# Kernel tuning notes

Hardware: AMD Instinct MI355X
Metric: run time of the kernel (lower is better)

Reference implementation:

```python
import jax, jax.numpy as jnp
import numpy as np

IN_DIM = 128
OUT_DIM = 128
N_NODES = 10000
N_EDGES = 640000


def setup_inputs() -> dict:
    key = jax.random.key(0)
    ks = jax.random.split(key, 9)
    X = jax.random.normal(ks[0], (N_NODES, IN_DIM), dtype=jnp.float32)
    edge_index = jax.random.randint(ks[1], (2, N_EDGES), 0, N_NODES, dtype=jnp.int64)
    edge_types = jax.random.randint(ks[2], (N_EDGES,), 0, 2, dtype=jnp.int64)
    s = 1.0 / np.sqrt(IN_DIM)
    W_data = jax.random.uniform(ks[3], (OUT_DIM, IN_DIM), minval=-s, maxval=s, dtype=jnp.float32)
    b_data = jax.random.uniform(ks[4], (OUT_DIM,), minval=-s, maxval=s, dtype=jnp.float32)
    W_control = jax.random.uniform(ks[5], (OUT_DIM, IN_DIM), minval=-s, maxval=s, dtype=jnp.float32)
    b_control = jax.random.uniform(ks[6], (OUT_DIM,), minval=-s, maxval=s, dtype=jnp.float32)
    W_self = jax.random.uniform(ks[7], (OUT_DIM, IN_DIM), minval=-s, maxval=s, dtype=jnp.float32)
    b_self = jax.random.uniform(ks[8], (OUT_DIM,), minval=-s, maxval=s, dtype=jnp.float32)
    return {"X": X, "edge_index": edge_index, "edge_types": edge_types,
            "W_data": W_data, "b_data": b_data,
            "W_control": W_control, "b_control": b_control,
            "W_self": W_self, "b_self": b_self}


def reference(X, edge_index, edge_types, W_data, b_data, W_control, b_control, W_self, b_self):
    src, dst = edge_index[0], edge_index[1]
    Xs = X[src]                               # [E, in_dim] gather
    m_data = Xs @ W_data.T + b_data           # [E, out_dim]
    m_ctrl = Xs @ W_control.T + b_control     # [E, out_dim]
    msg = jnp.where((edge_types == 0)[:, None], m_data, m_ctrl)
    agg = jax.ops.segment_sum(msg, dst, num_segments=X.shape[0])  # scatter-add to dst
    out = agg + (X @ W_self.T + b_self)
    return jax.nn.relu(out)
```

## Files before the change

kernel.cpp:

```cpp
#include <hip/hip_runtime.h>


#define IN_DIM 128
#define K_CAT  384
#define CAP    256
#define CSTR   16
#define ROWP   392

typedef short short8  __attribute__((ext_vector_type(8)));
typedef float floatx4 __attribute__((ext_vector_type(4)));

#define NW_ITEMS (8 * 12 * 64)

__device__ inline unsigned short f2bf(float f) {
    unsigned u = __float_as_uint(f);
    u += 0x7FFF + ((u >> 16) & 1);
    return (unsigned short)(u >> 16);
}
__device__ inline float bu2f(unsigned short h) {
    return __uint_as_float(((unsigned)h) << 16);
}

__global__ __launch_bounds__(256) void prep_kernel(
    const float* __restrict__ X,
    const float* __restrict__ Wd, const float* __restrict__ Wc,
    const float* __restrict__ Ws,
    unsigned short* __restrict__ WB,
    unsigned short* __restrict__ Xb,
    int* __restrict__ cnt, int N)
{
    const int NX = N * 32;
    const int NC = N * CSTR / 4;
    int idx = blockIdx.x * 256 + threadIdx.x;

    if (idx < NW_ITEMS) {
        int lane = idx & 63;
        int kt   = (idx >> 6) % 12;
        int nt   = idx / (64 * 12);
        int col  = nt * 16 + (lane & 15);
        int kb   = kt * 32 + (lane >> 4) * 8;
        unsigned short v[8];
        #pragma unroll
        for (int j = 0; j < 8; j++) {
            int k = kb + j;
            float w = (k < 128) ? Wd[col * 128 + k]
                    : (k < 256) ? Wc[col * 128 + (k - 128)]
                                : Ws[col * 128 + (k - 256)];
            v[j] = f2bf(w);
        }
        *(short8*)(WB + (size_t)idx * 8) = *(short8*)v;
        return;
    }
    idx -= NW_ITEMS;
    if (idx < NX) {
        float4 v = ((const float4*)X)[idx];
        ushort4 o;
        o.x = f2bf(v.x); o.y = f2bf(v.y); o.z = f2bf(v.z); o.w = f2bf(v.w);
        ((ushort4*)Xb)[idx] = o;
        return;
    }
    idx -= NX;
    if (idx < NC) {
        ((int4*)cnt)[idx] = make_int4(0, 0, 0, 0);
    }
}

__global__ __launch_bounds__(256) void append_kernel(
    const int* __restrict__ src,
    const int* __restrict__ dst,
    const int* __restrict__ etype,
    int* __restrict__ cnt,
    unsigned short* __restrict__ bucket, int E)
{
    int e = blockIdx.x * 256 + threadIdx.x;
    if (e >= E) return;
    int d = dst[e];
    int pos = atomicAdd(&cnt[d * CSTR], 1);
    if (pos < CAP) {
        bucket[(size_t)d * CAP + pos] =
            (unsigned short)(src[e] | (etype[e] << 15));
    }
}

__global__ __launch_bounds__(512) void fused_kernel(
    const unsigned short* __restrict__ Xb,
    const int* __restrict__ cnt,
    const unsigned short* __restrict__ bucket,
    const unsigned short* __restrict__ WB,
    const float* __restrict__ bd, const float* __restrict__ bc,
    const float* __restrict__ bs,
    float* __restrict__ out, int N)
{
    __shared__ unsigned short Als[16][ROWP];
    __shared__ float lc0[16], lc1[16];

    const int tid = threadIdx.x;
    const int m0  = blockIdx.x * 16;

    {
        const int hw = tid >> 5;
        const int q  = tid & 31;
        const int d  = m0 + hw;
        if (d < N) {
            const ushort4* Xb4 = (const ushort4*)Xb;
            int len = cnt[d * CSTR];
            if (len > CAP) len = CAP;

            float4 a0 = make_float4(0.f, 0.f, 0.f, 0.f);
            float4 a1 = make_float4(0.f, 0.f, 0.f, 0.f);
            int n0 = 0;
            const unsigned short* bl = bucket + (size_t)d * CAP;

#define PROC(P) do {                                                     \
            int _p = (int)(P);                                           \
            int _s = _p & 0x7FFF;                                        \
            int _t = _p >> 15;                                           \
            ushort4 _u = Xb4[_s * 32 + q];                               \
            float _x = bu2f(_u.x), _y = bu2f(_u.y);                      \
            float _z = bu2f(_u.z), _w = bu2f(_u.w);                      \
            float _m0 = _t ? 0.f : 1.f;                                  \
            float _m1 = 1.f - _m0;                                       \
            a0.x = fmaf(_x, _m0, a0.x); a1.x = fmaf(_x, _m1, a1.x);      \
            a0.y = fmaf(_y, _m0, a0.y); a1.y = fmaf(_y, _m1, a1.y);      \
            a0.z = fmaf(_z, _m0, a0.z); a1.z = fmaf(_z, _m1, a1.z);      \
            a0.w = fmaf(_w, _m0, a0.w); a1.w = fmaf(_w, _m1, a1.w);      \
            n0 += 1 - _t;                                                \
        } while (0)
#define PROC8(PP) do {                                                   \
            PROC((PP).x & 0xFFFF); PROC((PP).x >> 16);                   \
            PROC((PP).y & 0xFFFF); PROC((PP).y >> 16);                   \
            PROC((PP).z & 0xFFFF); PROC((PP).z >> 16);                   \
            PROC((PP).w & 0xFFFF); PROC((PP).w >> 16);                   \
        } while (0)

            int i = 0;
            for (; i + 16 <= len; i += 16) {
                uint4 p0 = *(const uint4*)(bl + i);
                uint4 p1 = *(const uint4*)(bl + i + 8);
                PROC8(p0); PROC8(p1);
            }
            for (; i + 8 <= len; i += 8) {
                uint4 p0 = *(const uint4*)(bl + i);
                PROC8(p0);
            }
            for (; i < len; i++) PROC(bl[i]);
#undef PROC8
#undef PROC

            ushort4 ux = Xb4[d * 32 + q];
            unsigned short* row = &Als[hw][0];
            ushort4 o;
            o.x = f2bf(a0.x); o.y = f2bf(a0.y); o.z = f2bf(a0.z); o.w = f2bf(a0.w);
            *(ushort4*)(row + q * 4) = o;
            o.x = f2bf(a1.x); o.y = f2bf(a1.y); o.z = f2bf(a1.z); o.w = f2bf(a1.w);
            *(ushort4*)(row + 128 + q * 4) = o;
            *(ushort4*)(row + 256 + q * 4) = ux;
            if (q == 0) {
                lc0[hw] = (float)n0;
                lc1[hw] = (float)(len - n0);
            }
        }
    }
    __syncthreads();

    const int wave = tid >> 6;
    const int lane = tid & 63;
    const int rA   = lane & 15;
    const int quad = lane >> 4;

    floatx4 acc = (floatx4){0.f, 0.f, 0.f, 0.f};
    const short8* B8 = (const short8*)WB + (size_t)wave * 12 * 64 + lane;

    #pragma unroll
    for (int kt = 0; kt < 12; kt++) {
        short8 a = *(const short8*)&Als[rA][kt * 32 + quad * 8];
        short8 b = B8[kt * 64];
        acc = __builtin_amdgcn_mfma_f32_16x16x32_bf16(a, b, acc, 0, 0, 0);
    }

    const int col = wave * 16 + rA;
    const float bdv = bd[col], bcv = bc[col], bsv = bs[col];
    #pragma unroll
    for (int r = 0; r < 4; r++) {
        int lrow = quad * 4 + r;
        int grow = m0 + lrow;
        if (grow < N) {
            float v = acc[r] + lc0[lrow] * bdv + lc1[lrow] * bcv + bsv;
            out[(size_t)grow * 128 + col] = fmaxf(v, 0.f);
        }
    }
}

extern "C" void kernel_launch(void* const* d_in, const int* in_sizes, int n_in,
                              void* d_out, int out_size, void* d_ws, size_t ws_size,
                              hipStream_t stream) {
    const float* X  = (const float*)d_in[0];
    const int*   ei = (const int*)d_in[1];
    const int*   et = (const int*)d_in[2];
    const float* Wd = (const float*)d_in[3];
    const float* bd = (const float*)d_in[4];
    const float* Wc = (const float*)d_in[5];
    const float* bc = (const float*)d_in[6];
    const float* Ws = (const float*)d_in[7];
    const float* bs = (const float*)d_in[8];
    float* out = (float*)d_out;

    const int N = in_sizes[0] / IN_DIM;
    const int E = in_sizes[2];

    unsigned short* WB     = (unsigned short*)d_ws;
    unsigned short* Xb     = WB + (size_t)NW_ITEMS * 8;
    unsigned short* bucket = Xb + (size_t)N * IN_DIM;
    int*            cnt    = (int*)(bucket + (size_t)N * CAP);

    const int* src = ei;
    const int* dst = ei + E;

    int prep_items = NW_ITEMS + N * 32 + N * CSTR / 4;
    prep_kernel<<<(prep_items + 255) / 256, 256, 0, stream>>>(
        X, Wd, Wc, Ws, WB, Xb, cnt, N);

    int eb = (E + 255) / 256;
    append_kernel<<<eb, 256, 0, stream>>>(src, dst, et, cnt, bucket, E);

    int fb = (N + 15) / 16;
    fused_kernel<<<fb, 512, 0, stream>>>(Xb, cnt, bucket, WB, bd, bc, bs, out, N);
}
```

Before: 131.5 us.

## Split edge buckets by type and gather with per-type half-warps

Edges now go into two per-destination buckets, one per edge type, each with its own counter, so the gather no longer needs masked dual accumulation. Each destination row is handled by two 16-thread groups, one per type. Each thread loads 16 bytes (8 bf16 values) per neighbour and accumulates with plain adds. The append kernel handles four edges per thread using vectorized loads. The cost is twice the bucket memory and a separate counter per type. Bucket capacity now applies per type, so truncation behaviour differs from before.

```diff
diff --git a/kernel.cpp b/kernel.cpp
--- a/kernel.cpp
+++ b/kernel.cpp
@@ -8,6 +8,7 @@
 #define ROWP   392
 
 typedef short short8  __attribute__((ext_vector_type(8)));
+typedef unsigned short ushortx8 __attribute__((ext_vector_type(8)));
 typedef float floatx4 __attribute__((ext_vector_type(4)));
 
 #define NW_ITEMS (8 * 12 * 64)
@@ -16,9 +17,6 @@
     unsigned u = __float_as_uint(f);
     u += 0x7FFF + ((u >> 16) & 1);
     return (unsigned short)(u >> 16);
-}
-__device__ inline float bu2f(unsigned short h) {
-    return __uint_as_float(((unsigned)h) << 16);
 }
 
 __global__ __launch_bounds__(256) void prep_kernel(
@@ -70,22 +68,39 @@
     const int* __restrict__ dst,
     const int* __restrict__ etype,
     int* __restrict__ cnt,
-    unsigned short* __restrict__ bucket, int E)
+    unsigned short* __restrict__ b0,
+    unsigned short* __restrict__ b1, int E)
 {
-    int e = blockIdx.x * 256 + threadIdx.x;
-    if (e >= E) return;
-    int d = dst[e];
-    int pos = atomicAdd(&cnt[d * CSTR], 1);
-    if (pos < CAP) {
-        bucket[(size_t)d * CAP + pos] =
-            (unsigned short)(src[e] | (etype[e] << 15));
-    }
+    int e0 = (blockIdx.x * 256 + threadIdx.x) * 4;
+
+#define PUT(SS, DD, TT) do {                                             \
+        int _d = (DD); int _t = (TT);                                    \
+        unsigned short* _b = _t ? b1 : b0;                               \
+        int _pos = atomicAdd(&cnt[_d * CSTR + (_t << 3)], 1);            \
+        if (_pos < CAP)                                                  \
+            _b[(size_t)_d * CAP + _pos] = (unsigned short)(SS);          \
+    } while (0)
+
+    if (e0 + 4 <= E) {
+        int4 s = *(const int4*)(src + e0);
+        int4 d = *(const int4*)(dst + e0);
+        int4 t = *(const int4*)(etype + e0);
+        PUT(s.x, d.x, t.x);
+        PUT(s.y, d.y, t.y);
+        PUT(s.z, d.z, t.z);
+        PUT(s.w, d.w, t.w);
+    } else {
+        for (int e = e0; e < E; e++)
+            PUT(src[e], dst[e], etype[e]);
+    }
+#undef PUT
 }
 
 __global__ __launch_bounds__(512) void fused_kernel(
     const unsigned short* __restrict__ Xb,
     const int* __restrict__ cnt,
-    const unsigned short* __restrict__ bucket,
+    const unsigned short* __restrict__ bucket0,
+    const unsigned short* __restrict__ bucket1,
     const unsigned short* __restrict__ WB,
     const float* __restrict__ bd, const float* __restrict__ bc,
     const float* __restrict__ bs,
@@ -98,66 +113,68 @@
     const int m0  = blockIdx.x * 16;
 
     {
-        const int hw = tid >> 5;
-        const int q  = tid & 31;
-        const int d  = m0 + hw;
+        const int hw2 = tid >> 4;
+        const int hw  = hw2 >> 1;
+        const int h   = hw2 & 1;
+        const int q   = tid & 15;
+        const int d   = m0 + hw;
         if (d < N) {
-            const ushort4* Xb4 = (const ushort4*)Xb;
-            int len = cnt[d * CSTR];
+            const uint4* Xr = (const uint4*)Xb;
+            int len = cnt[d * CSTR + (h << 3)];
             if (len > CAP) len = CAP;
-
-            float4 a0 = make_float4(0.f, 0.f, 0.f, 0.f);
-            float4 a1 = make_float4(0.f, 0.f, 0.f, 0.f);
-            int n0 = 0;
-            const unsigned short* bl = bucket + (size_t)d * CAP;
-
-#define PROC(P) do {                                                     \
-            int _p = (int)(P);                                           \
-            int _s = _p & 0x7FFF;                                        \
-            int _t = _p >> 15;                                           \
-            ushort4 _u = Xb4[_s * 32 + q];                               \
-            float _x = bu2f(_u.x), _y = bu2f(_u.y);                      \
-            float _z = bu2f(_u.z), _w = bu2f(_u.w);                      \
-            float _m0 = _t ? 0.f : 1.f;                                  \
-            float _m1 = 1.f - _m0;                                       \
-            a0.x = fmaf(_x, _m0, a0.x); a1.x = fmaf(_x, _m1, a1.x);      \
-            a0.y = fmaf(_y, _m0, a0.y); a1.y = fmaf(_y, _m1, a1.y);      \
-            a0.z = fmaf(_z, _m0, a0.z); a1.z = fmaf(_z, _m1, a1.z);      \
-            a0.w = fmaf(_w, _m0, a0.w); a1.w = fmaf(_w, _m1, a1.w);      \
-            n0 += 1 - _t;                                                \
+            const unsigned short* bl =
+                (h ? bucket1 : bucket0) + (size_t)d * CAP;
+
+            float a[8];
+            #pragma unroll
+            for (int j = 0; j < 8; j++) a[j] = 0.f;
+
+#define ACC(S) do {                                                      \
+            int _s = (int)(S);                                           \
+            uint4 _u = Xr[_s * 16 + q];                                  \
+            a[0] += __uint_as_float(_u.x << 16);                         \
+            a[1] += __uint_as_float(_u.x & 0xFFFF0000u);                 \
+            a[2] += __uint_as_float(_u.y << 16);                         \
+            a[3] += __uint_as_float(_u.y & 0xFFFF0000u);                 \
+            a[4] += __uint_as_float(_u.z << 16);                         \
+            a[5] += __uint_as_float(_u.z & 0xFFFF0000u);                 \
+            a[6] += __uint_as_float(_u.w << 16);                         \
+            a[7] += __uint_as_float(_u.w & 0xFFFF0000u);                 \
         } while (0)
-#define PROC8(PP) do {                                                   \
-            PROC((PP).x & 0xFFFF); PROC((PP).x >> 16);                   \
-            PROC((PP).y & 0xFFFF); PROC((PP).y >> 16);                   \
-            PROC((PP).z & 0xFFFF); PROC((PP).z >> 16);                   \
-            PROC((PP).w & 0xFFFF); PROC((PP).w >> 16);                   \
+#define ACC8(PP) do {                                                    \
+            ACC((PP).x & 0xFFFF); ACC((PP).x >> 16);                     \
+            ACC((PP).y & 0xFFFF); ACC((PP).y >> 16);                     \
+            ACC((PP).z & 0xFFFF); ACC((PP).z >> 16);                     \
+            ACC((PP).w & 0xFFFF); ACC((PP).w >> 16);                     \
         } while (0)
 
             int i = 0;
             for (; i + 16 <= len; i += 16) {
                 uint4 p0 = *(const uint4*)(bl + i);
                 uint4 p1 = *(const uint4*)(bl + i + 8);
-                PROC8(p0); PROC8(p1);
+                ACC8(p0); ACC8(p1);
             }
             for (; i + 8 <= len; i += 8) {
                 uint4 p0 = *(const uint4*)(bl + i);
-                PROC8(p0);
-            }
-            for (; i < len; i++) PROC(bl[i]);
-#undef PROC8
-#undef PROC
-
-            ushort4 ux = Xb4[d * 32 + q];
+                ACC8(p0);
+            }
+            for (; i < len; i++) ACC(bl[i]);
+#undef ACC8
+#undef ACC
+
             unsigned short* row = &Als[hw][0];
-            ushort4 o;
-            o.x = f2bf(a0.x); o.y = f2bf(a0.y); o.z = f2bf(a0.z); o.w = f2bf(a0.w);
-            *(ushort4*)(row + q * 4) = o;
-            o.x = f2bf(a1.x); o.y = f2bf(a1.y); o.z = f2bf(a1.z); o.w = f2bf(a1.w);
-            *(ushort4*)(row + 128 + q * 4) = o;
-            *(ushort4*)(row + 256 + q * 4) = ux;
+            ushortx8 o;
+            #pragma unroll
+            for (int j = 0; j < 8; j++) o[j] = f2bf(a[j]);
+            *(ushortx8*)(row + h * 128 + q * 8) = o;
+
+            if (h == 0) {
+                uint4 su = Xr[d * 16 + q];
+                *(uint4*)(row + 256 + q * 8) = su;
+            }
             if (q == 0) {
-                lc0[hw] = (float)n0;
-                lc1[hw] = (float)(len - n0);
+                if (h == 0) lc0[hw] = (float)len;
+                else        lc1[hw] = (float)len;
             }
         }
     }
@@ -208,10 +225,11 @@
     const int N = in_sizes[0] / IN_DIM;
     const int E = in_sizes[2];
 
-    unsigned short* WB     = (unsigned short*)d_ws;
-    unsigned short* Xb     = WB + (size_t)NW_ITEMS * 8;
-    unsigned short* bucket = Xb + (size_t)N * IN_DIM;
-    int*            cnt    = (int*)(bucket + (size_t)N * CAP);
+    unsigned short* WB  = (unsigned short*)d_ws;
+    unsigned short* Xb  = WB + (size_t)NW_ITEMS * 8;
+    unsigned short* b0  = Xb + (size_t)N * IN_DIM;
+    unsigned short* b1  = b0 + (size_t)N * CAP;
+    int*            cnt = (int*)(b1 + (size_t)N * CAP);
 
     const int* src = ei;
     const int* dst = ei + E;
@@ -220,9 +238,9 @@
     prep_kernel<<<(prep_items + 255) / 256, 256, 0, stream>>>(
         X, Wd, Wc, Ws, WB, Xb, cnt, N);
 
-    int eb = (E + 255) / 256;
-    append_kernel<<<eb, 256, 0, stream>>>(src, dst, et, cnt, bucket, E);
+    int eb = (E / 4 + 255) / 256;
+    append_kernel<<<eb, 256, 0, stream>>>(src, dst, et, cnt, b0, b1, E);
 
     int fb = (N + 15) / 16;
-    fused_kernel<<<fb, 512, 0, stream>>>(Xb, cnt, bucket, WB, bd, bc, bs, out, N);
-}
+    fused_kernel<<<fb, 512, 0, stream>>>(Xb, cnt, b0, b1, WB, bd, bc, bs, out, N);
+}
```

Measured after the change: 132.3 us. Within noise of the previous version (+0.6%).
